# Kernel optimization log

Measured on AMD Instinct MI355X. Metric: run time of the kernel, lower is better.

Reference implementation:

```python
import jax, jax.numpy as jnp
import numpy as np

N, F_IN, H, C = 100000, 256, 128, 64
E, EP = 1600000, 500000


def setup_inputs() -> dict:
    key = jax.random.key(0)
    ks = jax.random.split(key, 8)
    x = jax.random.normal(ks[0], (N, F_IN), jnp.float32)
    masked_nodes = jax.random.randint(ks[1], (1000,), 0, N)
    pos_edge_index = jax.random.randint(ks[2], (2, EP), 0, N)
    neg_edge_index = jax.random.randint(ks[3], (2, EP), 0, N)
    edge_index = jax.random.randint(ks[4], (2, E), 0, N)
    W1 = jax.random.normal(ks[5], (F_IN, H), jnp.float32) / np.sqrt(F_IN).astype(np.float32)
    b1 = jnp.zeros((H,), jnp.float32)
    W2 = jax.random.normal(ks[6], (H, C), jnp.float32) / np.sqrt(H).astype(np.float32)
    b2 = jnp.zeros((C,), jnp.float32)
    return dict(x=x, masked_nodes=masked_nodes, pos_edge_index=pos_edge_index,
                neg_edge_index=neg_edge_index, edge_index=edge_index,
                W1=W1, b1=b1, W2=W2, b2=b2)


def gcn_conv(x, W, b, src, dst, n):
    # PyG GCNConv: h = x @ W; symmetric norm with self-loops; aggregate; + bias
    h = x @ W  # [N, out]
    deg = jax.ops.segment_sum(jnp.ones(src.shape[0], h.dtype), dst, num_segments=n) + 1.0
    dis = jax.lax.rsqrt(deg)  # D^{-1/2} including self-loop
    msg = h[src] * (dis[src] * dis[dst])[:, None]           # gather + edge-norm
    agg = jax.ops.segment_sum(msg, dst, num_segments=n)      # scatter-add
    agg = agg + h * (dis * dis)[:, None]                      # self-loop term
    return agg + b


def reference(x, masked_nodes, pos_edge_index, neg_edge_index, edge_index, W1, b1, W2, b2):
    n = x.shape[0]
    src, dst = edge_index[0], edge_index[1]
    h = jax.nn.relu(gcn_conv(x, W1, b1, src, dst, n))
    h = gcn_conv(h, W2, b2, src, dst, n)  # [N, C]
    tei = jnp.concatenate([pos_edge_index, neg_edge_index], axis=-1)  # [2, 2*EP]
    x_j = h[tei[0]]  # [2EP, C]
    x_i = h[tei[1]]
    scores = jnp.einsum('ef,ef->e', x_i, x_j)
    return scores, jnp.zeros(tei.shape, jnp.float32)
```

## Files before the change

### kernel.cpp

```cpp
#include <hip/hip_runtime.h>

#define N_NODES 100000
#define F_IN    256
#define H_DIM   128
#define C_DIM   64
#define E_EDGES 1600000
#define EP_EDGES 500000

#define NBUK 391
#define EPB  4096

typedef unsigned short bf16_t;
typedef short  short8  __attribute__((ext_vector_type(8)));
typedef float  float4v __attribute__((ext_vector_type(4)));

__device__ inline bf16_t f2bf(float f) {
    unsigned u = __float_as_uint(f);
    u += 0x7fff + ((u >> 16) & 1);
    return (bf16_t)(u >> 16);
}
__device__ inline float bf2f(bf16_t h) {
    return __uint_as_float(((unsigned)h) << 16);
}
__device__ inline void split8(const float* vv, short* h, short* l) {
#pragma unroll
    for (int j = 0; j < 8; ++j) {
        bf16_t hb = f2bf(vv[j]);
        h[j] = (short)hb;
        l[j] = (short)f2bf(vv[j] - bf2f(hb));
    }
}
__device__ inline float4v mfma16(short8 a, short8 b, float4v c) {
    return __builtin_amdgcn_mfma_f32_16x16x32_bf16(a, b, c, 0, 0, 0);
}

__global__ __launch_bounds__(256) void bhist_kernel(const int* __restrict__ dst,
                                                    int* __restrict__ bsize) {
    __shared__ int hist[NBUK];
    const int t = threadIdx.x;
    for (int b = t; b < NBUK; b += 256) hist[b] = 0;
    __syncthreads();
    const int e0 = blockIdx.x * EPB;
#pragma unroll
    for (int i = 0; i < 16; ++i) {
        int e = e0 + i * 256 + t;
        if (e < E_EDGES) atomicAdd(&hist[dst[e] >> 8], 1);
    }
    __syncthreads();
    for (int b = t; b < NBUK; b += 256)
        if (hist[b]) atomicAdd(&bsize[b], hist[b]);
}

__global__ __launch_bounds__(512) void bscan_kernel(const int* __restrict__ bsize,
                                                    int* __restrict__ bbase,
                                                    int* __restrict__ bcursor) {
    __shared__ int sh[512];
    int t = threadIdx.x;
    sh[t] = (t < NBUK) ? bsize[t] : 0;
    __syncthreads();
#pragma unroll
    for (int off = 1; off < 512; off <<= 1) {
        int u = (t >= off) ? sh[t - off] : 0;
        __syncthreads();
        sh[t] += u;
        __syncthreads();
    }
    if (t < NBUK) {
        int ex = (t == 0) ? 0 : sh[t - 1];
        bbase[t] = ex;
        bcursor[t] = ex;
    }
    if (t == 0) bbase[NBUK] = E_EDGES;
}

__global__ __launch_bounds__(256) void bucket_scatter_kernel(const int* __restrict__ src,
                                                             const int* __restrict__ dst,
                                                             int* __restrict__ bcursor,
                                                             int2* __restrict__ pairs) {
    __shared__ int hist[NBUK];
    __shared__ int base[NBUK];
    const int t = threadIdx.x;
    for (int b = t; b < NBUK; b += 256) hist[b] = 0;
    __syncthreads();

    const int e0 = blockIdx.x * EPB;
    int s[16], d[16];
#pragma unroll
    for (int i = 0; i < 16; ++i) {
        int e = e0 + i * 256 + t;
        if (e < E_EDGES) {
            s[i] = src[e];
            d[i] = dst[e];
            atomicAdd(&hist[d[i] >> 8], 1);
        } else {
            d[i] = -1;
        }
    }
    __syncthreads();
    for (int b = t; b < NBUK; b += 256) {
        int c = hist[b];
        base[b] = c ? atomicAdd(&bcursor[b], c) : 0;
        hist[b] = 0;
    }
    __syncthreads();
#pragma unroll
    for (int i = 0; i < 16; ++i) {
        if (d[i] >= 0) {
            int b = d[i] >> 8;
            int r = atomicAdd(&hist[b], 1);
            pairs[base[b] + r] = make_int2(s[i], d[i]);
        }
    }
}

__global__ __launch_bounds__(256) void bucket_sort_kernel(const int2* __restrict__ pairs,
                                                          const int* __restrict__ bbase,
                                                          int* __restrict__ row_ptr,
                                                          float* __restrict__ dis,
                                                          int* __restrict__ csr_src) {
    __shared__ int cnt[256];
    __shared__ int sh[256];
    __shared__ int cur[256];
    const int b = blockIdx.x;
    const int node0 = b << 8;
    const int t = threadIdx.x;
    const int nn = min(256, N_NODES - node0);
    const int beg = bbase[b], end = bbase[b + 1];
    cnt[t] = 0;
    __syncthreads();
    for (int e = beg + t; e < end; e += 256)
        atomicAdd(&cnt[pairs[e].y - node0], 1);
    __syncthreads();
    int c = cnt[t];
    if (t < nn) dis[node0 + t] = rsqrtf((float)c + 1.0f);
    sh[t] = c;
    __syncthreads();
#pragma unroll
    for (int off = 1; off < 256; off <<= 1) {
        int u = (t >= off) ? sh[t - off] : 0;
        __syncthreads();
        sh[t] += u;
        __syncthreads();
    }
    int start = beg + sh[t] - c;
    if (t < nn) row_ptr[node0 + t] = start;
    cur[t] = start;
    if (b == NBUK - 1 && t == 0) row_ptr[N_NODES] = E_EDGES;
    __syncthreads();
    for (int e = beg + t; e < end; e += 256) {
        int2 p = pairs[e];
        int j = atomicAdd(&cur[p.y - node0], 1);
        csr_src[j] = p.x;
    }
}

__global__ __launch_bounds__(256) void wprep_kernel(const float* __restrict__ W1,
                                                    const float* __restrict__ W2,
                                                    short* __restrict__ w1h,
                                                    short* __restrict__ w1l,
                                                    short* __restrict__ w2h,
                                                    short* __restrict__ w2l) {
    int idx = blockIdx.x * 256 + threadIdx.x;
    if (idx < H_DIM * F_IN) {
        int n = idx >> 8, k = idx & 255;
        float w = W1[k * H_DIM + n];
        bf16_t h = f2bf(w);
        w1h[idx] = (short)h;
        w1l[idx] = (short)f2bf(w - bf2f(h));
    }
    int i2 = idx - H_DIM * F_IN;
    if (i2 >= 0 && i2 < C_DIM * H_DIM) {
        int n = i2 >> 7, k = i2 & 127;
        float w = W2[k * C_DIM + n];
        bf16_t h = f2bf(w);
        w2h[i2] = (short)h;
        w2l[i2] = (short)f2bf(w - bf2f(h));
    }
}

#define LSTR 40
__global__ __launch_bounds__(256, 3) void gemm1_mfma(const float* __restrict__ X,
                                                     const short* __restrict__ Wth,
                                                     const short* __restrict__ Wtl,
                                                     bf16_t* __restrict__ T,
                                                     int nrows) {
    __shared__ short Bh[128 * LSTR], Bl[128 * LSTR];
    const int t = threadIdx.x;
    const int row0 = blockIdx.x * 128;
    const int w = t >> 6;
    const int lane = t & 63;
    const int m = lane & 15;
    const int q = lane >> 4;
    const int koff = q * 8;

    const int r0 = row0 + w * 32 + m;
    const int r1 = r0 + 16;
    const bool ok0 = r0 < nrows;
    const bool ok1 = r1 < nrows;
    const float* X0 = X + (long long)r0 * F_IN + q * 8;
    const float* X1 = X + (long long)r1 * F_IN + q * 8;

    float4v acc[2][8];
#pragma unroll
    for (int i = 0; i < 2; ++i)
#pragma unroll
        for (int j = 0; j < 8; ++j) acc[i][j] = {0.f, 0.f, 0.f, 0.f};

#pragma unroll 2
    for (int ks = 0; ks < 8; ++ks) {
        const int k0 = ks * 32;
#pragma unroll
        for (int i = 0; i < 2; ++i) {
            int c = t + i * 256;
            int n = c >> 2, kc = c & 3;
            *(short8*)&Bh[n * LSTR + kc * 8] = *(const short8*)&Wth[n * F_IN + k0 + kc * 8];
            *(short8*)&Bl[n * LSTR + kc * 8] = *(const short8*)&Wtl[n * F_IN + k0 + kc * 8];
        }
        float a0[8] = {0.f, 0.f, 0.f, 0.f, 0.f, 0.f, 0.f, 0.f};
        float a1[8] = {0.f, 0.f, 0.f, 0.f, 0.f, 0.f, 0.f, 0.f};
        if (ok0) {
            *(float4*)&a0[0] = *(const float4*)&X0[k0];
            *(float4*)&a0[4] = *(const float4*)&X0[k0 + 4];
        }
        if (ok1) {
            *(float4*)&a1[0] = *(const float4*)&X1[k0];
            *(float4*)&a1[4] = *(const float4*)&X1[k0 + 4];
        }
        short8 ah0, al0, ah1, al1;
        split8(a0, (short*)&ah0, (short*)&al0);
        split8(a1, (short*)&ah1, (short*)&al1);
        __syncthreads();
#pragma unroll
        for (int nc = 0; nc < 8; ++nc) {
            short8 bh = *(const short8*)&Bh[(nc * 16 + m) * LSTR + koff];
            short8 bl = *(const short8*)&Bl[(nc * 16 + m) * LSTR + koff];
            acc[0][nc] = mfma16(ah0, bh, acc[0][nc]);
            acc[0][nc] = mfma16(al0, bh, acc[0][nc]);
            acc[0][nc] = mfma16(ah0, bl, acc[0][nc]);
            acc[1][nc] = mfma16(ah1, bh, acc[1][nc]);
            acc[1][nc] = mfma16(al1, bh, acc[1][nc]);
            acc[1][nc] = mfma16(ah1, bl, acc[1][nc]);
        }
        __syncthreads();
    }
#pragma unroll
    for (int mt = 0; mt < 2; ++mt)
#pragma unroll
        for (int nc = 0; nc < 8; ++nc)
#pragma unroll
            for (int reg = 0; reg < 4; ++reg) {
                int grow = row0 + w * 32 + mt * 16 + q * 4 + reg;
                int gcol = nc * 16 + m;
                if (grow < nrows)
                    T[(long long)grow * H_DIM + gcol] = f2bf(acc[mt][nc][reg]);
            }
}

__global__ __launch_bounds__(256) void gemm2_mfma(const float* __restrict__ A,
                                                  const float* __restrict__ b1,
                                                  const short* __restrict__ Wth,
                                                  const short* __restrict__ Wtl,
                                                  bf16_t* __restrict__ T,
                                                  int nrows) {
    __shared__ short Bh[64 * LSTR], Bl[64 * LSTR];
    const int t = threadIdx.x;
    const int row0 = blockIdx.x * 128;
    const int w = t >> 6;
    const int lane = t & 63;
    const int m = lane & 15;
    const int q = lane >> 4;
    const int koff = q * 8;

    const int r0 = row0 + w * 32 + m;
    const int r1 = r0 + 16;
    const bool ok0 = r0 < nrows;
    const bool ok1 = r1 < nrows;
    const float* A0 = A + (long long)r0 * H_DIM + q * 8;
    const float* A1 = A + (long long)r1 * H_DIM + q * 8;
    const float* bp = b1 + q * 8;

    float4v acc[2][4];
#pragma unroll
    for (int i = 0; i < 2; ++i)
#pragma unroll
        for (int j = 0; j < 4; ++j) acc[i][j] = {0.f, 0.f, 0.f, 0.f};

#pragma unroll 2
    for (int ks = 0; ks < 4; ++ks) {
        const int k0 = ks * 32;
        {
            int n = t >> 2, kc = t & 3;
            *(short8*)&Bh[n * LSTR + kc * 8] = *(const short8*)&Wth[n * H_DIM + k0 + kc * 8];
            *(short8*)&Bl[n * LSTR + kc * 8] = *(const short8*)&Wtl[n * H_DIM + k0 + kc * 8];
        }
        float4 bv0 = *(const float4*)&bp[k0];
        float4 bv1 = *(const float4*)&bp[k0 + 4];
        float a0[8] = {0.f, 0.f, 0.f, 0.f, 0.f, 0.f, 0.f, 0.f};
        float a1[8] = {0.f, 0.f, 0.f, 0.f, 0.f, 0.f, 0.f, 0.f};
        if (ok0) {
            float4 v0 = *(const float4*)&A0[k0];
            float4 v1 = *(const float4*)&A0[k0 + 4];
            a0[0] = fmaxf(v0.x + bv0.x, 0.f); a0[1] = fmaxf(v0.y + bv0.y, 0.f);
            a0[2] = fmaxf(v0.z + bv0.z, 0.f); a0[3] = fmaxf(v0.w + bv0.w, 0.f);
            a0[4] = fmaxf(v1.x + bv1.x, 0.f); a0[5] = fmaxf(v1.y + bv1.y, 0.f);
            a0[6] = fmaxf(v1.z + bv1.z, 0.f); a0[7] = fmaxf(v1.w + bv1.w, 0.f);
        }
        if (ok1) {
            float4 v0 = *(const float4*)&A1[k0];
            float4 v1 = *(const float4*)&A1[k0 + 4];
            a1[0] = fmaxf(v0.x + bv0.x, 0.f); a1[1] = fmaxf(v0.y + bv0.y, 0.f);
            a1[2] = fmaxf(v0.z + bv0.z, 0.f); a1[3] = fmaxf(v0.w + bv0.w, 0.f);
            a1[4] = fmaxf(v1.x + bv1.x, 0.f); a1[5] = fmaxf(v1.y + bv1.y, 0.f);
            a1[6] = fmaxf(v1.z + bv1.z, 0.f); a1[7] = fmaxf(v1.w + bv1.w, 0.f);
        }
        short8 ah0, al0, ah1, al1;
        split8(a0, (short*)&ah0, (short*)&al0);
        split8(a1, (short*)&ah1, (short*)&al1);
        __syncthreads();
#pragma unroll
        for (int nc = 0; nc < 4; ++nc) {
            short8 bh = *(const short8*)&Bh[(nc * 16 + m) * LSTR + koff];
            short8 bl = *(const short8*)&Bl[(nc * 16 + m) * LSTR + koff];
            acc[0][nc] = mfma16(ah0, bh, acc[0][nc]);
            acc[0][nc] = mfma16(al0, bh, acc[0][nc]);
            acc[0][nc] = mfma16(ah0, bl, acc[0][nc]);
            acc[1][nc] = mfma16(ah1, bh, acc[1][nc]);
            acc[1][nc] = mfma16(al1, bh, acc[1][nc]);
            acc[1][nc] = mfma16(ah1, bl, acc[1][nc]);
        }
        __syncthreads();
    }
#pragma unroll
    for (int mt = 0; mt < 2; ++mt)
#pragma unroll
        for (int nc = 0; nc < 4; ++nc)
#pragma unroll
            for (int reg = 0; reg < 4; ++reg) {
                int grow = row0 + w * 32 + mt * 16 + q * 4 + reg;
                int gcol = nc * 16 + m;
                if (grow < nrows)
                    T[(long long)grow * C_DIM + gcol] = f2bf(acc[mt][nc][reg]);
            }
}

__device__ inline void fma8_bf16(float* acc, uint4 u, float c) {
#pragma unroll
    for (int p = 0; p < 4; ++p) {
        unsigned w = (&u.x)[p];
        float lo = __uint_as_float(w << 16);
        float hi = __uint_as_float(w & 0xffff0000u);
        acc[2 * p]     = fmaf(lo, c, acc[2 * p]);
        acc[2 * p + 1] = fmaf(hi, c, acc[2 * p + 1]);
    }
}

template <int CS, bool HAS_BIAS>
__global__ __launch_bounds__(256) void agg_kernel(const bf16_t* __restrict__ t,
                                                  const float* __restrict__ dis,
                                                  const int* __restrict__ row_ptr,
                                                  const int* __restrict__ csr_src,
                                                  const float* __restrict__ bias,
                                                  float* __restrict__ agg) {
    unsigned idx = blockIdx.x * 256u + threadIdx.x;
    if (idx >= (unsigned)(N_NODES << CS)) return;
    int node = idx >> CS;
    int q = idx & ((1 << CS) - 1);
    const uint4* tv = (const uint4*)t;
    float dd = dis[node];
    int beg = row_ptr[node], end = row_ptr[node + 1];

    float acc[8];
#pragma unroll
    for (int p = 0; p < 8; ++p) acc[p] = 0.0f;
    fma8_bf16(acc, tv[idx], dd * dd);

    int j = beg;
    for (; j + 3 < end; j += 4) {
        int s0 = csr_src[j + 0], s1 = csr_src[j + 1];
        int s2 = csr_src[j + 2], s3 = csr_src[j + 3];
        float c0 = dis[s0] * dd, c1 = dis[s1] * dd;
        float c2 = dis[s2] * dd, c3 = dis[s3] * dd;
        uint4 u0 = tv[((unsigned)s0 << CS) + q];
        uint4 u1 = tv[((unsigned)s1 << CS) + q];
        uint4 u2 = tv[((unsigned)s2 << CS) + q];
        uint4 u3 = tv[((unsigned)s3 << CS) + q];
        fma8_bf16(acc, u0, c0);
        fma8_bf16(acc, u1, c1);
        fma8_bf16(acc, u2, c2);
        fma8_bf16(acc, u3, c3);
    }
    for (; j < end; ++j) {
        int s = csr_src[j];
        float c = dis[s] * dd;
        fma8_bf16(acc, tv[((unsigned)s << CS) + q], c);
    }

    if (HAS_BIAS) {
        float4 bv0 = ((const float4*)bias)[q * 2];
        float4 bv1 = ((const float4*)bias)[q * 2 + 1];
        acc[0] += bv0.x; acc[1] += bv0.y; acc[2] += bv0.z; acc[3] += bv0.w;
        acc[4] += bv1.x; acc[5] += bv1.y; acc[6] += bv1.z; acc[7] += bv1.w;
    }
    float4 o0 = make_float4(acc[0], acc[1], acc[2], acc[3]);
    float4 o1 = make_float4(acc[4], acc[5], acc[6], acc[7]);
    ((float4*)agg)[idx * 2]     = o0;
    ((float4*)agg)[idx * 2 + 1] = o1;
}

__global__ __launch_bounds__(256) void score_kernel(const float* __restrict__ h2,
                                                    const int* __restrict__ pos,
                                                    const int* __restrict__ neg,
                                                    float* __restrict__ out) {
    int tid = blockIdx.x * 256 + threadIdx.x;
    int e = tid >> 4;
    int q = tid & 15;
    if (e >= 2 * EP_EDGES) return;
    int i, j;
    if (e < EP_EDGES) {
        j = pos[e];
        i = pos[EP_EDGES + e];
    } else {
        j = neg[e - EP_EDGES];
        i = neg[e];
    }
    float4 a = ((const float4*)h2)[i * (C_DIM / 4) + q];
    float4 b = ((const float4*)h2)[j * (C_DIM / 4) + q];
    float v = a.x * b.x + a.y * b.y + a.z * b.z + a.w * b.w;
    v += __shfl_down(v, 8, 16);
    v += __shfl_down(v, 4, 16);
    v += __shfl_down(v, 2, 16);
    v += __shfl_down(v, 1, 16);
    if (q == 0) out[e] = v;
}

extern "C" void kernel_launch(void* const* d_in, const int* in_sizes, int n_in,
                              void* d_out, int out_size, void* d_ws, size_t ws_size,
                              hipStream_t stream) {
    const float* x  = (const float*)d_in[0];
    const int* pos  = (const int*)d_in[2];
    const int* neg  = (const int*)d_in[3];
    const int* ei   = (const int*)d_in[4];
    const float* W1 = (const float*)d_in[5];
    const float* b1 = (const float*)d_in[6];
    const float* W2 = (const float*)d_in[7];
    const float* b2 = (const float*)d_in[8];
    float* out = (float*)d_out;

    char* ws = (char*)d_ws;
    float*  dis     = (float*) (ws + 0);
    int*    row_ptr = (int*)   (ws + 400000);
    int*    bsize   = (int*)   (ws + 800128);
    int*    bbase   = (int*)   (ws + 801792);
    int*    bcursor = (int*)   (ws + 803456);
    int*    csr_src = (int*)   (ws + 805120);
    int2*   pairs   = (int2*)  (ws + 7205120);
    bf16_t* t       = (bf16_t*)(ws + 20005120);
    float*  agg     = (float*) (ws + 45605120);
    short*  w1th    = (short*) (ws + 96805120);
    short*  w1tl    = (short*) (ws + 96870656);
    short*  w2th    = (short*) (ws + 96936192);
    short*  w2tl    = (short*) (ws + 96952576);

    const int* esrc = ei;
    const int* edst = ei + E_EDGES;

    hipMemsetAsync(bsize, 0, NBUK * sizeof(int), stream);
    bhist_kernel<<<(E_EDGES + EPB - 1) / EPB, 256, 0, stream>>>(edst, bsize);
    bscan_kernel<<<1, 512, 0, stream>>>(bsize, bbase, bcursor);
    bucket_scatter_kernel<<<(E_EDGES + EPB - 1) / EPB, 256, 0, stream>>>(
        esrc, edst, bcursor, pairs);
    bucket_sort_kernel<<<NBUK, 256, 0, stream>>>(pairs, bbase, row_ptr, dis, csr_src);
    wprep_kernel<<<(H_DIM * F_IN + C_DIM * H_DIM + 255) / 256, 256, 0, stream>>>(
        W1, W2, w1th, w1tl, w2th, w2tl);

    gemm1_mfma<<<(N_NODES + 127) / 128, 256, 0, stream>>>(x, w1th, w1tl, t, N_NODES);
    agg_kernel<4, false><<<(N_NODES * 16 + 255) / 256, 256, 0, stream>>>(
        t, dis, row_ptr, csr_src, nullptr, agg);

    gemm2_mfma<<<(N_NODES + 127) / 128, 256, 0, stream>>>(agg, b1, w2th, w2tl, t, N_NODES);
    agg_kernel<3, true><<<(N_NODES * 8 + 255) / 256, 256, 0, stream>>>(
        t, dis, row_ptr, csr_src, b2, agg);

    score_kernel<<<(2 * EP_EDGES * 16) / 256, 256, 0, stream>>>(agg, pos, neg, out);

    hipMemsetAsync(out + 2 * EP_EDGES, 0, (size_t)4 * EP_EDGES * sizeof(float), stream);
}
```

Before: 435.6 us.

## Fold source-side degree norm into GEMM epilogue and store layer-2 output in fp16

The GEMM epilogues now scale each row by dis[row], so the aggregation kernels only sum neighbour rows and multiply once by dis[node] at the end. This removes a random dis[src] gather and an fma per edge in both aggregation passes. The second aggregation writes its output as fp16 into the old pairs buffer, and the score kernel reads half-width rows with 8 lanes per edge, halving gather traffic in scoring. The cost is an extra rounding step on the final embeddings.

```diff
diff --git a/kernel.cpp b/kernel.cpp
--- a/kernel.cpp
+++ b/kernel.cpp
@@ -13,6 +13,7 @@
 typedef unsigned short bf16_t;
 typedef short  short8  __attribute__((ext_vector_type(8)));
 typedef float  float4v __attribute__((ext_vector_type(4)));
+typedef _Float16 half8v __attribute__((ext_vector_type(8)));
 
 __device__ inline bf16_t f2bf(float f) {
     unsigned u = __float_as_uint(f);
@@ -182,6 +183,7 @@
 __global__ __launch_bounds__(256, 3) void gemm1_mfma(const float* __restrict__ X,
                                                      const short* __restrict__ Wth,
                                                      const short* __restrict__ Wtl,
+                                                     const float* __restrict__ dis,
                                                      bf16_t* __restrict__ T,
                                                      int nrows) {
     __shared__ short Bh[128 * LSTR], Bl[128 * LSTR];
@@ -243,6 +245,14 @@
         }
         __syncthreads();
     }
+    float ds[2][4];
+#pragma unroll
+    for (int mt = 0; mt < 2; ++mt)
+#pragma unroll
+        for (int reg = 0; reg < 4; ++reg) {
+            int grow = row0 + w * 32 + mt * 16 + q * 4 + reg;
+            ds[mt][reg] = (grow < nrows) ? dis[grow] : 0.f;
+        }
 #pragma unroll
     for (int mt = 0; mt < 2; ++mt)
 #pragma unroll
@@ -252,7 +262,7 @@
                 int grow = row0 + w * 32 + mt * 16 + q * 4 + reg;
                 int gcol = nc * 16 + m;
                 if (grow < nrows)
-                    T[(long long)grow * H_DIM + gcol] = f2bf(acc[mt][nc][reg]);
+                    T[(long long)grow * H_DIM + gcol] = f2bf(acc[mt][nc][reg] * ds[mt][reg]);
             }
 }
 
@@ -260,6 +270,7 @@
                                                   const float* __restrict__ b1,
                                                   const short* __restrict__ Wth,
                                                   const short* __restrict__ Wtl,
+                                                  const float* __restrict__ dis,
                                                   bf16_t* __restrict__ T,
                                                   int nrows) {
     __shared__ short Bh[64 * LSTR], Bl[64 * LSTR];
@@ -330,6 +341,14 @@
         }
         __syncthreads();
     }
+    float ds[2][4];
+#pragma unroll
+    for (int mt = 0; mt < 2; ++mt)
+#pragma unroll
+        for (int reg = 0; reg < 4; ++reg) {
+            int grow = row0 + w * 32 + mt * 16 + q * 4 + reg;
+            ds[mt][reg] = (grow < nrows) ? dis[grow] : 0.f;
+        }
 #pragma unroll
     for (int mt = 0; mt < 2; ++mt)
 #pragma unroll
@@ -339,61 +358,66 @@
                 int grow = row0 + w * 32 + mt * 16 + q * 4 + reg;
                 int gcol = nc * 16 + m;
                 if (grow < nrows)
-                    T[(long long)grow * C_DIM + gcol] = f2bf(acc[mt][nc][reg]);
+                    T[(long long)grow * C_DIM + gcol] = f2bf(acc[mt][nc][reg] * ds[mt][reg]);
             }
 }
 
-__device__ inline void fma8_bf16(float* acc, uint4 u, float c) {
+__device__ inline void add8_bf16(float* acc, uint4 u) {
 #pragma unroll
     for (int p = 0; p < 4; ++p) {
         unsigned w = (&u.x)[p];
-        float lo = __uint_as_float(w << 16);
-        float hi = __uint_as_float(w & 0xffff0000u);
-        acc[2 * p]     = fmaf(lo, c, acc[2 * p]);
-        acc[2 * p + 1] = fmaf(hi, c, acc[2 * p + 1]);
-    }
-}
-
-template <int CS, bool HAS_BIAS>
+        acc[2 * p]     += __uint_as_float(w << 16);
+        acc[2 * p + 1] += __uint_as_float(w & 0xffff0000u);
+    }
+}
+
+template <int CS, bool HAS_BIAS, bool F16OUT>
 __global__ __launch_bounds__(256) void agg_kernel(const bf16_t* __restrict__ t,
                                                   const float* __restrict__ dis,
                                                   const int* __restrict__ row_ptr,
                                                   const int* __restrict__ csr_src,
                                                   const float* __restrict__ bias,
-                                                  float* __restrict__ agg) {
+                                                  float* __restrict__ aggf,
+                                                  _Float16* __restrict__ aggh) {
     unsigned idx = blockIdx.x * 256u + threadIdx.x;
     if (idx >= (unsigned)(N_NODES << CS)) return;
     int node = idx >> CS;
     int q = idx & ((1 << CS) - 1);
     const uint4* tv = (const uint4*)t;
-    float dd = dis[node];
     int beg = row_ptr[node], end = row_ptr[node + 1];
 
     float acc[8];
-#pragma unroll
-    for (int p = 0; p < 8; ++p) acc[p] = 0.0f;
-    fma8_bf16(acc, tv[idx], dd * dd);
+    {
+        uint4 u = tv[idx];
+#pragma unroll
+        for (int p = 0; p < 4; ++p) {
+            unsigned w = (&u.x)[p];
+            acc[2 * p]     = __uint_as_float(w << 16);
+            acc[2 * p + 1] = __uint_as_float(w & 0xffff0000u);
+        }
+    }
 
     int j = beg;
     for (; j + 3 < end; j += 4) {
         int s0 = csr_src[j + 0], s1 = csr_src[j + 1];
         int s2 = csr_src[j + 2], s3 = csr_src[j + 3];
-        float c0 = dis[s0] * dd, c1 = dis[s1] * dd;
-        float c2 = dis[s2] * dd, c3 = dis[s3] * dd;
         uint4 u0 = tv[((unsigned)s0 << CS) + q];
         uint4 u1 = tv[((unsigned)s1 << CS) + q];
         uint4 u2 = tv[((unsigned)s2 << CS) + q];
         uint4 u3 = tv[((unsigned)s3 << CS) + q];
-        fma8_bf16(acc, u0, c0);
-        fma8_bf16(acc, u1, c1);
-        fma8_bf16(acc, u2, c2);
-        fma8_bf16(acc, u3, c3);
+        add8_bf16(acc, u0);
+        add8_bf16(acc, u1);
+        add8_bf16(acc, u2);
+        add8_bf16(acc, u3);
     }
     for (; j < end; ++j) {
         int s = csr_src[j];
-        float c = dis[s] * dd;
-        fma8_bf16(acc, tv[((unsigned)s << CS) + q], c);
-    }
+        add8_bf16(acc, tv[((unsigned)s << CS) + q]);
+    }
+
+    float dd = dis[node];
+#pragma unroll
+    for (int p = 0; p < 8; ++p) acc[p] *= dd;
 
     if (HAS_BIAS) {
         float4 bv0 = ((const float4*)bias)[q * 2];
@@ -401,19 +425,26 @@
         acc[0] += bv0.x; acc[1] += bv0.y; acc[2] += bv0.z; acc[3] += bv0.w;
         acc[4] += bv1.x; acc[5] += bv1.y; acc[6] += bv1.z; acc[7] += bv1.w;
     }
-    float4 o0 = make_float4(acc[0], acc[1], acc[2], acc[3]);
-    float4 o1 = make_float4(acc[4], acc[5], acc[6], acc[7]);
-    ((float4*)agg)[idx * 2]     = o0;
-    ((float4*)agg)[idx * 2 + 1] = o1;
-}
-
-__global__ __launch_bounds__(256) void score_kernel(const float* __restrict__ h2,
+    if (F16OUT) {
+        half8v hv;
+#pragma unroll
+        for (int p = 0; p < 8; ++p) hv[p] = (_Float16)acc[p];
+        ((half8v*)aggh)[idx] = hv;
+    } else {
+        float4 o0 = make_float4(acc[0], acc[1], acc[2], acc[3]);
+        float4 o1 = make_float4(acc[4], acc[5], acc[6], acc[7]);
+        ((float4*)aggf)[idx * 2]     = o0;
+        ((float4*)aggf)[idx * 2 + 1] = o1;
+    }
+}
+
+__global__ __launch_bounds__(256) void score_kernel(const _Float16* __restrict__ h2,
                                                     const int* __restrict__ pos,
                                                     const int* __restrict__ neg,
                                                     float* __restrict__ out) {
     int tid = blockIdx.x * 256 + threadIdx.x;
-    int e = tid >> 4;
-    int q = tid & 15;
+    int e = tid >> 3;
+    int q = tid & 7;
     if (e >= 2 * EP_EDGES) return;
     int i, j;
     if (e < EP_EDGES) {
@@ -423,13 +454,14 @@
         j = neg[e - EP_EDGES];
         i = neg[e];
     }
-    float4 a = ((const float4*)h2)[i * (C_DIM / 4) + q];
-    float4 b = ((const float4*)h2)[j * (C_DIM / 4) + q];
-    float v = a.x * b.x + a.y * b.y + a.z * b.z + a.w * b.w;
-    v += __shfl_down(v, 8, 16);
-    v += __shfl_down(v, 4, 16);
-    v += __shfl_down(v, 2, 16);
-    v += __shfl_down(v, 1, 16);
+    half8v a = ((const half8v*)h2)[i * 8 + q];
+    half8v b = ((const half8v*)h2)[j * 8 + q];
+    float v = 0.f;
+#pragma unroll
+    for (int k = 0; k < 8; ++k) v = fmaf((float)a[k], (float)b[k], v);
+    v += __shfl_down(v, 4, 8);
+    v += __shfl_down(v, 2, 8);
+    v += __shfl_down(v, 1, 8);
     if (q == 0) out[e] = v;
 }
 
@@ -454,6 +486,7 @@
     int*    bcursor = (int*)   (ws + 803456);
     int*    csr_src = (int*)   (ws + 805120);
     int2*   pairs   = (int2*)  (ws + 7205120);
+    _Float16* h2f16 = (_Float16*)(ws + 7205120);
     bf16_t* t       = (bf16_t*)(ws + 20005120);
     float*  agg     = (float*) (ws + 45605120);
     short*  w1th    = (short*) (ws + 96805120);
@@ -473,15 +506,15 @@
     wprep_kernel<<<(H_DIM * F_IN + C_DIM * H_DIM + 255) / 256, 256, 0, stream>>>(
         W1, W2, w1th, w1tl, w2th, w2tl);
 
-    gemm1_mfma<<<(N_NODES + 127) / 128, 256, 0, stream>>>(x, w1th, w1tl, t, N_NODES);
-    agg_kernel<4, false><<<(N_NODES * 16 + 255) / 256, 256, 0, stream>>>(
-        t, dis, row_ptr, csr_src, nullptr, agg);
-
-    gemm2_mfma<<<(N_NODES + 127) / 128, 256, 0, stream>>>(agg, b1, w2th, w2tl, t, N_NODES);
-    agg_kernel<3, true><<<(N_NODES * 8 + 255) / 256, 256, 0, stream>>>(
-        t, dis, row_ptr, csr_src, b2, agg);
-
-    score_kernel<<<(2 * EP_EDGES * 16) / 256, 256, 0, stream>>>(agg, pos, neg, out);
+    gemm1_mfma<<<(N_NODES + 127) / 128, 256, 0, stream>>>(x, w1th, w1tl, dis, t, N_NODES);
+    agg_kernel<4, false, false><<<(N_NODES * 16 + 255) / 256, 256, 0, stream>>>(
+        t, dis, row_ptr, csr_src, nullptr, agg, nullptr);
+
+    gemm2_mfma<<<(N_NODES + 127) / 128, 256, 0, stream>>>(agg, b1, w2th, w2tl, dis, t, N_NODES);
+    agg_kernel<3, true, true><<<(N_NODES * 8 + 255) / 256, 256, 0, stream>>>(
+        t, dis, row_ptr, csr_src, b2, nullptr, h2f16);
+
+    score_kernel<<<(2 * EP_EDGES * 8) / 256, 256, 0, stream>>>(h2f16, pos, neg, out);
 
     hipMemsetAsync(out + 2 * EP_EDGES, 0, (size_t)4 * EP_EDGES * sizeof(float), stream);
 }
```

New measurement: 403.3 us. 1.08x faster.
